# Kernel tuning notes

Hardware: AMD Instinct MI355X
Metric: run time of the kernel (lower is better)

Reference implementation:

```python
import jax, jax.numpy as jnp
import numpy as np

B, T, C, H = 32, 576, 1024, 16
D = C // H  # head_dim = 64

def setup_inputs() -> dict:
    key = jax.random.key(0)
    ks = jax.random.split(key, 5)
    s = 1.0 / np.sqrt(C)
    return {
        "emb_img": jax.random.normal(ks[0], (B, T, C), dtype=jnp.float32),
        "w_qkv": jax.random.normal(ks[1], (C, 3 * C), dtype=jnp.float32) * s,
        "b_qkv": jnp.zeros((3 * C,), dtype=jnp.float32),
        "w_proj": jax.random.normal(ks[2], (C, C), dtype=jnp.float32) * s,
        "b_proj": jnp.zeros((C,), dtype=jnp.float32),
    }

def reference(emb_img, w_qkv, b_qkv, w_proj, b_proj):
    # fused QKV projection
    qkv = emb_img @ w_qkv + b_qkv                       # [B,T,3C]
    q, k, v = jnp.split(qkv, 3, axis=-1)                # each [B,T,C]
    def heads(x):
        return x.reshape(B, T, H, D).transpose(0, 2, 1, 3)  # [B,H,T,D]
    q, k, v = heads(q), heads(k), heads(v)
    # note: original scales by 1/head_dim (not 1/sqrt(head_dim))
    scores = jnp.einsum("bhqd,bhkd->bhqk", q, k) * (1.0 / D)
    causal = jnp.tril(jnp.ones((T, T), dtype=bool))
    scores = jnp.where(causal[None, None], scores, -jnp.inf)
    att = jax.nn.softmax(scores, axis=-1)               # [B,H,T,T]
    y = jnp.einsum("bhqk,bhkd->bhqd", att, v)           # [B,H,T,D]
    y = y.transpose(0, 2, 1, 3).reshape(B, T, C)
    return y @ w_proj + b_proj
```

## Files before the change

kernel.cpp:

```cpp
#include <hip/hip_runtime.h>
#include <stdint.h>

namespace {

constexpr int kB = 32, kT = 576, kC = 1024, kH = 16, kD = 64;
constexpr int kM = kB * kT;
constexpr int kNqkv = 3 * kC;

typedef uint16_t u16;
typedef __attribute__((ext_vector_type(4))) float f32x4;
typedef __attribute__((ext_vector_type(8))) short short8;
typedef __attribute__((ext_vector_type(8))) __bf16 bf16x8;
typedef __attribute__((ext_vector_type(4))) uint16_t u16x4;

#define VMCNT(n) asm volatile("s_waitcnt vmcnt(" #n ")" ::: "memory")

__device__ __forceinline__ f32x4 mfma_bf16(short8 a, short8 b, f32x4 c) {
  return __builtin_amdgcn_mfma_f32_16x16x32_bf16(
      __builtin_bit_cast(bf16x8, a), __builtin_bit_cast(bf16x8, b), c, 0, 0, 0);
}

__device__ __forceinline__ u16 to_bf16(float x) {
  uint32_t u = __float_as_uint(x);
  u += 0x7fffu + ((u >> 16) & 1u);
  return (u16)(u >> 16);
}

__device__ __forceinline__ void gload_lds16(const void* g, void* l) {
  __builtin_amdgcn_global_load_lds(
      (const __attribute__((address_space(1))) uint32_t*)(uintptr_t)g,
      (__attribute__((address_space(3))) uint32_t*)(uintptr_t)l,
      16, 0, 0);
}

__device__ __forceinline__ void bar() {
  asm volatile("" ::: "memory");
  __builtin_amdgcn_s_barrier();
  asm volatile("" ::: "memory");
}

__global__ __launch_bounds__(256) void cvt_bf16_kernel(
    const float* __restrict__ in, u16* __restrict__ out, int n4) {
  const int i = blockIdx.x * 256 + threadIdx.x;
  if (i >= n4) return;
  const f32x4 v = ((const f32x4*)in)[i];
  u16x4 o;
#pragma unroll
  for (int j = 0; j < 4; ++j) o[j] = to_bf16(v[j]);
  ((u16x4*)out)[i] = o;
}

__global__ void tconv_kernel(const float* __restrict__ in, u16* __restrict__ out,
                             int K, int N) {
  __shared__ u16 tile[32][33];
  const int nb = blockIdx.x * 32;
  const int kb = blockIdx.y * 32;
  const int tx = threadIdx.x;
  const int ty = threadIdx.y;
#pragma unroll
  for (int i = 0; i < 32; i += 8)
    tile[ty + i][tx] = to_bf16(in[(size_t)(kb + ty + i) * N + nb + tx]);
  __syncthreads();
#pragma unroll
  for (int i = 0; i < 32; i += 8)
    out[(size_t)(nb + ty + i) * K + kb + tx] = tile[tx][ty + i];
}

__global__ __launch_bounds__(512, 2) void gemm_qkv(
    const u16* __restrict__ A, const u16* __restrict__ Bt,
    const float* __restrict__ bias,
    u16* __restrict__ outQ, u16* __restrict__ outK, u16* __restrict__ outVT) {
  constexpr int Kc = 1024;
  constexpr int NT = Kc / 64;
  __shared__ char lds[3][49152];

  const int tid = threadIdx.x;
  const int wave = tid >> 6;
  const int lane = tid & 63;
  const int lo = lane & 15;
  const int hi = lane >> 4;
  const int wr = wave >> 2;
  const int wc = wave & 3;

  const int lin = blockIdx.x + blockIdx.y * 24;
  const int l2 = (lin & 7) * 216 + (lin >> 3);
  const int n0 = (l2 % 24) * 128;
  const int m0 = (l2 / 24) * 256;

  const u16* srcA[4];
  const u16* srcB[2];
#pragma unroll
  for (int c = 0; c < 4; ++c) {
    const int b = c * 8192 + wave * 1024 + lane * 16;
    const int row = b >> 7;
    const int colb = (b & 127) ^ ((row & 7) << 4);
    srcA[c] = A + (size_t)(m0 + row) * Kc + (colb >> 1);
  }
#pragma unroll
  for (int c = 0; c < 2; ++c) {
    const int b = c * 8192 + wave * 1024 + lane * 16;
    const int row = b >> 7;
    const int colb = (b & 127) ^ ((row & 7) << 4);
    srcB[c] = Bt + (size_t)(n0 + row) * Kc + (colb >> 1);
  }

  auto stage = [&](int slot, int t) {
    const int k0 = t * 64;
    char* base = &lds[slot][0];
#pragma unroll
    for (int c = 0; c < 4; ++c)
      gload_lds16(srcA[c] + k0, base + c * 8192 + wave * 1024);
#pragma unroll
    for (int c = 0; c < 2; ++c)
      gload_lds16(srcB[c] + k0, base + 32768 + c * 8192 + wave * 1024);
  };

  f32x4 acc[8][2] = {};

  auto compute = [&](int slot) {
    const char* base = &lds[slot][0];
    __builtin_amdgcn_s_setprio(1);
#pragma unroll
    for (int ks = 0; ks < 2; ++ks) {
      const int cb = (ks * 64 + hi * 16) ^ ((lo & 7) << 4);
      short8 af[8], bfv[2];
#pragma unroll
      for (int i = 0; i < 8; ++i)
        af[i] = *(const short8*)(base + (wr * 128 + i * 16 + lo) * 128 + cb);
#pragma unroll
      for (int j = 0; j < 2; ++j)
        bfv[j] = *(const short8*)(base + 32768 + (wc * 32 + j * 16 + lo) * 128 + cb);
#pragma unroll
      for (int i = 0; i < 8; ++i)
#pragma unroll
        for (int j = 0; j < 2; ++j)
          acc[i][j] = mfma_bf16(af[i], bfv[j], acc[i][j]);
    }
    __builtin_amdgcn_s_setprio(0);
  };

  stage(0, 0);
  stage(1, 1);
  for (int t = 0; t < NT - 2; ++t) {
    stage((t + 2) % 3, t + 2);
    VMCNT(12);
    bar();
    compute(t % 3);
    bar();
  }
  VMCNT(6);
  bar();
  compute((NT - 2) % 3);
  bar();
  VMCNT(0);
  bar();
  compute((NT - 1) % 3);

  if (n0 >= 2048) {
    bar();
    u16* wlds = (u16*)&lds[0][0] + wave * (32 * 132);
    uint32_t* wlds32 = (uint32_t*)wlds;
#pragma unroll
    for (int j = 0; j < 2; ++j) {
      const int n = n0 + wc * 32 + j * 16 + lo;
      const float bv = bias[n];
#pragma unroll
      for (int i = 0; i < 8; ++i)
#pragma unroll
        for (int rp = 0; rp < 2; ++rp) {
          const u16 w0 = to_bf16(acc[i][j][rp * 2] + bv);
          const u16 w1 = to_bf16(acc[i][j][rp * 2 + 1] + bv);
          wlds32[(j * 16 + lo) * 66 + i * 8 + hi * 2 + rp] =
              (uint32_t)w0 | ((uint32_t)w1 << 16);
        }
    }
    const int l32 = lane & 31;
    const int lh = lane >> 5;
#pragma unroll
    for (int p = 0; p < 16; ++p) {
      const int d_local = p * 2 + lh;
      const int n = n0 + wc * 32 + d_local;
      const int c = n & 1023;
      const int hh = c >> 6;
      const int d = c & 63;
      const int m = m0 + wr * 128 + l32 * 4;
      const int bb = m / kT;
      const int t = m - bb * kT;
      const u16x4 v = *(const u16x4*)&wlds[d_local * 132 + l32 * 4];
      *(u16x4*)&outVT[((size_t)(bb * kH + hh) * kD + d) * kT + t] = v;
    }
  } else {
#pragma unroll
    for (int j = 0; j < 2; ++j) {
      const int n = n0 + wc * 32 + j * 16 + lo;
      const float bv = bias[n];
      const int which = n >> 10;
      const int c = n & 1023;
      const int hh = c >> 6;
      const int d = c & 63;
#pragma unroll
      for (int i = 0; i < 8; ++i) {
        const int mrow = m0 + wr * 128 + i * 16 + hi * 4;
#pragma unroll
        for (int r = 0; r < 4; ++r) {
          const int m = mrow + r;
          const int bb = m / kT;
          const int t = m - bb * kT;
          const float v = acc[i][j][r] + bv;
          if (which == 0)
            outQ[((size_t)(bb * kH + hh) * kT + t) * kD + d] = to_bf16(v * (1.0f / 64.0f));
          else
            outK[((size_t)(bb * kH + hh) * kT + t) * kD + d] = to_bf16(v);
        }
      }
    }
  }
}

__global__ __launch_bounds__(256, 3) void gemm_proj(
    const u16* __restrict__ A, const u16* __restrict__ Bt,
    const float* __restrict__ bias, float* __restrict__ outF) {
  constexpr int Kc = 1024;
  constexpr int NT = Kc / 32;
  __shared__ char lds[3][16384];

  const int tid = threadIdx.x;
  const int wave = tid >> 6;
  const int lane = tid & 63;
  const int lo = lane & 15;
  const int hi = lane >> 4;
  const int wr = wave >> 1;
  const int wc = wave & 1;

  const int lin = blockIdx.x + blockIdx.y * 8;
  const int l2 = (lin & 7) * 144 + (lin >> 3);
  const int n0 = (l2 & 7) * 128;
  const int m0 = (l2 >> 3) * 128;

  const u16* srcA[2];
  const u16* srcB[2];
#pragma unroll
  for (int c = 0; c < 2; ++c) {
    const int off = c * 4096 + tid * 16;
    const int p = off >> 7;
    const int col = (off & 127) ^ ((p & 7) << 4);
    const int r_ = (col < 64) ? p : p + 64;
    const int k_ = (col & 63) >> 1;
    srcA[c] = A + (size_t)(m0 + r_) * Kc + k_;
    srcB[c] = Bt + (size_t)(n0 + r_) * Kc + k_;
  }

  auto stage = [&](int slot, int t) {
    char* base = &lds[slot][0];
#pragma unroll
    for (int c = 0; c < 2; ++c) {
      gload_lds16(srcA[c] + t * 32, base + c * 4096 + wave * 1024);
      gload_lds16(srcB[c] + t * 32, base + 8192 + c * 4096 + wave * 1024);
    }
  };

  f32x4 acc[4][4] = {};

  auto compute = [&](int slot) {
    const char* base = &lds[slot][0];
    const char* baseB = base + 8192;
    const int swz = (lo & 7) << 4;
    short8 af[4], bf[4];
#pragma unroll
    for (int i = 0; i < 4; ++i)
      af[i] = *(const short8*)(base + (i * 16 + lo) * 128 + ((wr * 64 + hi * 16) ^ swz));
#pragma unroll
    for (int j = 0; j < 4; ++j)
      bf[j] = *(const short8*)(baseB + (j * 16 + lo) * 128 + ((wc * 64 + hi * 16) ^ swz));
    __builtin_amdgcn_s_setprio(1);
#pragma unroll
    for (int i = 0; i < 4; ++i)
#pragma unroll
      for (int j = 0; j < 4; ++j)
        acc[i][j] = mfma_bf16(af[i], bf[j], acc[i][j]);
    __builtin_amdgcn_s_setprio(0);
  };

  stage(0, 0);
  stage(1, 1);
  for (int t = 0; t < NT - 2; ++t) {
    stage((t + 2) % 3, t + 2);
    VMCNT(8);
    bar();
    compute(t % 3);
    bar();
  }
  VMCNT(4);
  bar();
  compute((NT - 2) % 3);
  bar();
  VMCNT(0);
  bar();
  compute((NT - 1) % 3);

#pragma unroll
  for (int j = 0; j < 4; ++j) {
    const int n = n0 + wc * 64 + j * 16 + lo;
    const float bv = bias[n];
#pragma unroll
    for (int i = 0; i < 4; ++i) {
      const int mrow = m0 + wr * 64 + i * 16 + hi * 4;
#pragma unroll
      for (int r = 0; r < 4; ++r)
        outF[(size_t)(mrow + r) * kC + n] = acc[i][j][r] + bv;
    }
  }
}

__global__ __launch_bounds__(256) void attn_kernel(
    const u16* __restrict__ Q, const u16* __restrict__ K,
    const u16* __restrict__ VT, u16* __restrict__ Y) {
  __shared__ u16 P[4][32][72];

  const int bh = blockIdx.y;
  const int wave = threadIdx.x >> 6;
  const int lane = threadIdx.x & 63;
  const int lo = lane & 15;
  const int hi = lane >> 4;
  const int q0 = blockIdx.x * 128 + wave * 32;
  if (q0 >= kT) return;

  const u16* Qb = Q + (size_t)bh * kT * kD;
  const u16* Kb = K + (size_t)bh * kT * kD;
  const u16* Vb = VT + (size_t)bh * kD * kT;

  short8 qf[2][2];
#pragma unroll
  for (int h = 0; h < 2; ++h) {
    const u16* qp = Qb + (q0 + h * 16 + lo) * kD + hi * 8;
    qf[h][0] = *(const short8*)qp;
    qf[h][1] = *(const short8*)(qp + 32);
  }

  f32x4 acc[2][4] = {};
  float mrun[2][4], lrun[2][4];
#pragma unroll
  for (int h = 0; h < 2; ++h)
#pragma unroll
    for (int r = 0; r < 4; ++r) { mrun[h][r] = -3e38f; lrun[h][r] = 0.f; }

  const int kv_end = q0 + 32;
  for (int kv = 0; kv < kv_end; kv += 64) {
    f32x4 s[2][4];
#pragma unroll
    for (int kc = 0; kc < 4; ++kc) {
      const u16* kp = Kb + (kv + kc * 16 + lo) * kD + hi * 8;
      const short8 kf0 = *(const short8*)kp;
      const short8 kf1 = *(const short8*)(kp + 32);
#pragma unroll
      for (int h = 0; h < 2; ++h) {
        f32x4 z = {0.f, 0.f, 0.f, 0.f};
        z = mfma_bf16(qf[h][0], kf0, z);
        z = mfma_bf16(qf[h][1], kf1, z);
        s[h][kc] = z;
      }
    }
    if (kv + 63 > q0) {
#pragma unroll
      for (int h = 0; h < 2; ++h)
#pragma unroll
        for (int kc = 0; kc < 4; ++kc)
#pragma unroll
          for (int r = 0; r < 4; ++r)
            if (kv + kc * 16 + lo > q0 + h * 16 + hi * 4 + r) s[h][kc][r] = -3e38f;
    }
#pragma unroll
    for (int h = 0; h < 2; ++h) {
      float pm[4], rs[4], corr[4];
#pragma unroll
      for (int r = 0; r < 4; ++r)
        pm[r] = fmaxf(fmaxf(s[h][0][r], s[h][1][r]), fmaxf(s[h][2][r], s[h][3][r]));
#pragma unroll
      for (int off = 8; off >= 1; off >>= 1)
#pragma unroll
        for (int r = 0; r < 4; ++r) pm[r] = fmaxf(pm[r], __shfl_xor(pm[r], off));
#pragma unroll
      for (int r = 0; r < 4; ++r) {
        const float mnew = fmaxf(mrun[h][r], pm[r]);
        corr[r] = __expf(mrun[h][r] - mnew);
        mrun[h][r] = mnew;
      }
#pragma unroll
      for (int r = 0; r < 4; ++r) {
        float acc_rs = 0.f;
#pragma unroll
        for (int kc = 0; kc < 4; ++kc) {
          const float pv = __expf(s[h][kc][r] - mrun[h][r]);
          acc_rs += pv;
          P[wave][h * 16 + hi * 4 + r][kc * 16 + lo] = to_bf16(pv);
        }
        rs[r] = acc_rs;
      }
#pragma unroll
      for (int off = 8; off >= 1; off >>= 1)
#pragma unroll
        for (int r = 0; r < 4; ++r) rs[r] += __shfl_xor(rs[r], off);
#pragma unroll
      for (int r = 0; r < 4; ++r) lrun[h][r] = lrun[h][r] * corr[r] + rs[r];
#pragma unroll
      for (int nt = 0; nt < 4; ++nt)
#pragma unroll
        for (int r = 0; r < 4; ++r) acc[h][nt][r] *= corr[r];
    }
    short8 pf[2][2];
#pragma unroll
    for (int h = 0; h < 2; ++h) {
      pf[h][0] = *(const short8*)&P[wave][h * 16 + lo][hi * 8];
      pf[h][1] = *(const short8*)&P[wave][h * 16 + lo][32 + hi * 8];
    }
#pragma unroll
    for (int nt = 0; nt < 4; ++nt) {
      const u16* vp = Vb + (nt * 16 + lo) * kT + kv + hi * 8;
      const short8 vf0 = *(const short8*)vp;
      const short8 vf1 = *(const short8*)(vp + 32);
#pragma unroll
      for (int h = 0; h < 2; ++h) {
        acc[h][nt] = mfma_bf16(pf[h][0], vf0, acc[h][nt]);
        acc[h][nt] = mfma_bf16(pf[h][1], vf1, acc[h][nt]);
      }
    }
  }

  const int b = bh >> 4, hh = bh & 15;
#pragma unroll
  for (int h = 0; h < 2; ++h)
#pragma unroll
    for (int r = 0; r < 4; ++r) {
      const float inv = 1.0f / lrun[h][r];
      const int t = q0 + h * 16 + hi * 4 + r;
      const size_t base = ((size_t)(b * kT + t) * kH + hh) * kD;
#pragma unroll
      for (int nt = 0; nt < 4; ++nt)
        Y[base + nt * 16 + lo] = to_bf16(acc[h][nt][r] * inv);
    }
}

}

extern "C" void kernel_launch(void* const* d_in, const int* in_sizes, int n_in,
                              void* d_out, int out_size, void* d_ws, size_t ws_size,
                              hipStream_t stream) {
  (void)in_sizes; (void)n_in; (void)out_size; (void)ws_size;
  const float* emb   = (const float*)d_in[0];
  const float* wqkv  = (const float*)d_in[1];
  const float* bqkv  = (const float*)d_in[2];
  const float* wproj = (const float*)d_in[3];
  const float* bproj = (const float*)d_in[4];
  float* out = (float*)d_out;

  char* p = (char*)d_ws;
  u16* embb   = (u16*)p; p += (size_t)kM * kC * 2;
  u16* wqkvt  = (u16*)p; p += (size_t)kNqkv * kC * 2;
  u16* wprojt = (u16*)p; p += (size_t)kC * kC * 2;
  u16* Qh     = (u16*)p; p += (size_t)kM * kC * 2;
  u16* Kh     = (u16*)p; p += (size_t)kM * kC * 2;
  u16* VTh    = (u16*)p; p += (size_t)kM * kC * 2;
  u16* Yh     = (u16*)p; p += (size_t)kM * kC * 2;

  const int n4 = kM * kC / 4;
  cvt_bf16_kernel<<<dim3((n4 + 255) / 256), 256, 0, stream>>>(emb, embb, n4);
  tconv_kernel<<<dim3(kNqkv / 32, kC / 32), dim3(32, 8), 0, stream>>>(wqkv, wqkvt, kC, kNqkv);
  tconv_kernel<<<dim3(kC / 32, kC / 32), dim3(32, 8), 0, stream>>>(wproj, wprojt, kC, kC);
  gemm_qkv<<<dim3(kNqkv / 128, kM / 256), 512, 0, stream>>>(
      embb, wqkvt, bqkv, Qh, Kh, VTh);
  attn_kernel<<<dim3((kT + 127) / 128, kB * kH), 256, 0, stream>>>(Qh, Kh, VTh, Yh);
  gemm_proj<<<dim3(kC / 128, kM / 128), 256, 0, stream>>>(
      Yh, wprojt, bproj, out);
}
```

Baseline: 371.0 us.

## Restructure attention: transposed scores, exp2 softmax, K/V prefetch, heavy-first scheduling

Reworks the attention kernel in several ways. It computes S^T (K as the A operand), so each lane owns one query row and the row max/sum need only two cross-lane shuffles. The log2(e) factor is folded into the Q scale so exp2 can be used directly. Next-tile K fragments and current V fragments are loaded before the softmax to hide load latency, and the grid is flattened so the longest causal query blocks launch first. In exchange it uses more registers for the prefetched fragments and changes the P write pattern to LDS.

```diff
diff --git a/kernel.cpp b/kernel.cpp
--- a/kernel.cpp
+++ b/kernel.cpp
@@ -6,6 +6,7 @@
 constexpr int kB = 32, kT = 576, kC = 1024, kH = 16, kD = 64;
 constexpr int kM = kB * kT;
 constexpr int kNqkv = 3 * kC;
+constexpr float kQScale = 1.4426950408889634f / 64.0f;
 
 typedef uint16_t u16;
 typedef __attribute__((ext_vector_type(4))) float f32x4;
@@ -14,6 +15,10 @@
 typedef __attribute__((ext_vector_type(4))) uint16_t u16x4;
 
 #define VMCNT(n) asm volatile("s_waitcnt vmcnt(" #n ")" ::: "memory")
+
+__device__ __forceinline__ float fexp2(float x) {
+  return __builtin_amdgcn_exp2f(x);
+}
 
 __device__ __forceinline__ f32x4 mfma_bf16(short8 a, short8 b, f32x4 c) {
   return __builtin_amdgcn_mfma_f32_16x16x32_bf16(
@@ -208,7 +213,7 @@
           const int t = m - bb * kT;
           const float v = acc[i][j][r] + bv;
           if (which == 0)
-            outQ[((size_t)(bb * kH + hh) * kT + t) * kD + d] = to_bf16(v * (1.0f / 64.0f));
+            outQ[((size_t)(bb * kH + hh) * kT + t) * kD + d] = to_bf16(v * kQScale);
           else
             outK[((size_t)(bb * kH + hh) * kT + t) * kD + d] = to_bf16(v);
         }
@@ -317,12 +322,14 @@
     const u16* __restrict__ VT, u16* __restrict__ Y) {
   __shared__ u16 P[4][32][72];
 
-  const int bh = blockIdx.y;
+  const int idx = blockIdx.x;
+  const int qi = 4 - (idx >> 9);
+  const int bh = idx & 511;
   const int wave = threadIdx.x >> 6;
   const int lane = threadIdx.x & 63;
   const int lo = lane & 15;
   const int hi = lane >> 4;
-  const int q0 = blockIdx.x * 128 + wave * 32;
+  const int q0 = qi * 128 + wave * 32;
   if (q0 >= kT) return;
 
   const u16* Qb = Q + (size_t)bh * kT * kD;
@@ -338,74 +345,84 @@
   }
 
   f32x4 acc[2][4] = {};
-  float mrun[2][4], lrun[2][4];
-#pragma unroll
-  for (int h = 0; h < 2; ++h)
-#pragma unroll
-    for (int r = 0; r < 4; ++r) { mrun[h][r] = -3e38f; lrun[h][r] = 0.f; }
+  float mrun[2] = {-3e38f, -3e38f};
+  float lsum[2] = {0.f, 0.f};
+
+  short8 kf[4][2];
+#pragma unroll
+  for (int kc = 0; kc < 4; ++kc) {
+    const u16* kp = Kb + (kc * 16 + lo) * kD + hi * 8;
+    kf[kc][0] = *(const short8*)kp;
+    kf[kc][1] = *(const short8*)(kp + 32);
+  }
 
   const int kv_end = q0 + 32;
   for (int kv = 0; kv < kv_end; kv += 64) {
     f32x4 s[2][4];
 #pragma unroll
-    for (int kc = 0; kc < 4; ++kc) {
-      const u16* kp = Kb + (kv + kc * 16 + lo) * kD + hi * 8;
-      const short8 kf0 = *(const short8*)kp;
-      const short8 kf1 = *(const short8*)(kp + 32);
+    for (int kc = 0; kc < 4; ++kc)
 #pragma unroll
       for (int h = 0; h < 2; ++h) {
         f32x4 z = {0.f, 0.f, 0.f, 0.f};
-        z = mfma_bf16(qf[h][0], kf0, z);
-        z = mfma_bf16(qf[h][1], kf1, z);
+        z = mfma_bf16(kf[kc][0], qf[h][0], z);
+        z = mfma_bf16(kf[kc][1], qf[h][1], z);
         s[h][kc] = z;
       }
+    short8 vf[4][2];
+#pragma unroll
+    for (int nt = 0; nt < 4; ++nt) {
+      const u16* vp = Vb + (nt * 16 + lo) * kT + kv + hi * 8;
+      vf[nt][0] = *(const short8*)vp;
+      vf[nt][1] = *(const short8*)(vp + 32);
+    }
+    if (kv + 64 < kv_end) {
+#pragma unroll
+      for (int kc = 0; kc < 4; ++kc) {
+        const u16* kp = Kb + (kv + 64 + kc * 16 + lo) * kD + hi * 8;
+        kf[kc][0] = *(const short8*)kp;
+        kf[kc][1] = *(const short8*)(kp + 32);
+      }
     }
     if (kv + 63 > q0) {
 #pragma unroll
-      for (int h = 0; h < 2; ++h)
+      for (int h = 0; h < 2; ++h) {
+        const int q = q0 + h * 16 + lo;
 #pragma unroll
         for (int kc = 0; kc < 4; ++kc)
 #pragma unroll
           for (int r = 0; r < 4; ++r)
-            if (kv + kc * 16 + lo > q0 + h * 16 + hi * 4 + r) s[h][kc][r] = -3e38f;
+            if (kv + kc * 16 + hi * 4 + r > q) s[h][kc][r] = -3e38f;
+      }
     }
 #pragma unroll
     for (int h = 0; h < 2; ++h) {
-      float pm[4], rs[4], corr[4];
-#pragma unroll
-      for (int r = 0; r < 4; ++r)
-        pm[r] = fmaxf(fmaxf(s[h][0][r], s[h][1][r]), fmaxf(s[h][2][r], s[h][3][r]));
-#pragma unroll
-      for (int off = 8; off >= 1; off >>= 1)
-#pragma unroll
-        for (int r = 0; r < 4; ++r) pm[r] = fmaxf(pm[r], __shfl_xor(pm[r], off));
-#pragma unroll
-      for (int r = 0; r < 4; ++r) {
-        const float mnew = fmaxf(mrun[h][r], pm[r]);
-        corr[r] = __expf(mrun[h][r] - mnew);
-        mrun[h][r] = mnew;
-      }
-#pragma unroll
-      for (int r = 0; r < 4; ++r) {
-        float acc_rs = 0.f;
-#pragma unroll
-        for (int kc = 0; kc < 4; ++kc) {
-          const float pv = __expf(s[h][kc][r] - mrun[h][r]);
-          acc_rs += pv;
-          P[wave][h * 16 + hi * 4 + r][kc * 16 + lo] = to_bf16(pv);
+      float m01 = fmaxf(fmaxf(s[h][0][0], s[h][0][1]), fmaxf(s[h][0][2], s[h][0][3]));
+      float m23 = fmaxf(fmaxf(s[h][1][0], s[h][1][1]), fmaxf(s[h][1][2], s[h][1][3]));
+      float m45 = fmaxf(fmaxf(s[h][2][0], s[h][2][1]), fmaxf(s[h][2][2], s[h][2][3]));
+      float m67 = fmaxf(fmaxf(s[h][3][0], s[h][3][1]), fmaxf(s[h][3][2], s[h][3][3]));
+      float pm = fmaxf(fmaxf(m01, m23), fmaxf(m45, m67));
+      pm = fmaxf(pm, __shfl_xor(pm, 16));
+      pm = fmaxf(pm, __shfl_xor(pm, 32));
+      const float mnew = fmaxf(mrun[h], pm);
+      const float corr = fexp2(mrun[h] - mnew);
+      mrun[h] = mnew;
+      float psum = 0.f;
+#pragma unroll
+      for (int kc = 0; kc < 4; ++kc) {
+        u16x4 pk;
+#pragma unroll
+        for (int r = 0; r < 4; ++r) {
+          const float pv = fexp2(s[h][kc][r] - mnew);
+          psum += pv;
+          pk[r] = to_bf16(pv);
         }
-        rs[r] = acc_rs;
-      }
-#pragma unroll
-      for (int off = 8; off >= 1; off >>= 1)
-#pragma unroll
-        for (int r = 0; r < 4; ++r) rs[r] += __shfl_xor(rs[r], off);
-#pragma unroll
-      for (int r = 0; r < 4; ++r) lrun[h][r] = lrun[h][r] * corr[r] + rs[r];
+        *(u16x4*)&P[wave][h * 16 + lo][kc * 16 + hi * 4] = pk;
+      }
+      lsum[h] = lsum[h] * corr + psum;
 #pragma unroll
       for (int nt = 0; nt < 4; ++nt)
 #pragma unroll
-        for (int r = 0; r < 4; ++r) acc[h][nt][r] *= corr[r];
+        for (int r = 0; r < 4; ++r) acc[h][nt][r] *= corr;
     }
     short8 pf[2][2];
 #pragma unroll
@@ -414,29 +431,30 @@
       pf[h][1] = *(const short8*)&P[wave][h * 16 + lo][32 + hi * 8];
     }
 #pragma unroll
-    for (int nt = 0; nt < 4; ++nt) {
-      const u16* vp = Vb + (nt * 16 + lo) * kT + kv + hi * 8;
-      const short8 vf0 = *(const short8*)vp;
-      const short8 vf1 = *(const short8*)(vp + 32);
+    for (int nt = 0; nt < 4; ++nt)
 #pragma unroll
       for (int h = 0; h < 2; ++h) {
-        acc[h][nt] = mfma_bf16(pf[h][0], vf0, acc[h][nt]);
-        acc[h][nt] = mfma_bf16(pf[h][1], vf1, acc[h][nt]);
-      }
-    }
-  }
-
+        acc[h][nt] = mfma_bf16(pf[h][0], vf[nt][0], acc[h][nt]);
+        acc[h][nt] = mfma_bf16(pf[h][1], vf[nt][1], acc[h][nt]);
+      }
+  }
+
+#pragma unroll
+  for (int h = 0; h < 2; ++h) {
+    lsum[h] += __shfl_xor(lsum[h], 16);
+    lsum[h] += __shfl_xor(lsum[h], 32);
+  }
   const int b = bh >> 4, hh = bh & 15;
 #pragma unroll
   for (int h = 0; h < 2; ++h)
 #pragma unroll
     for (int r = 0; r < 4; ++r) {
-      const float inv = 1.0f / lrun[h][r];
+      const float linv = 1.0f / __shfl(lsum[h], hi * 4 + r);
       const int t = q0 + h * 16 + hi * 4 + r;
       const size_t base = ((size_t)(b * kT + t) * kH + hh) * kD;
 #pragma unroll
       for (int nt = 0; nt < 4; ++nt)
-        Y[base + nt * 16 + lo] = to_bf16(acc[h][nt][r] * inv);
+        Y[base + nt * 16 + lo] = to_bf16(acc[h][nt][r] * linv);
     }
 }
 
@@ -468,7 +486,7 @@
   tconv_kernel<<<dim3(kC / 32, kC / 32), dim3(32, 8), 0, stream>>>(wproj, wprojt, kC, kC);
   gemm_qkv<<<dim3(kNqkv / 128, kM / 256), 512, 0, stream>>>(
       embb, wqkvt, bqkv, Qh, Kh, VTh);
-  attn_kernel<<<dim3((kT + 127) / 128, kB * kH), 256, 0, stream>>>(Qh, Kh, VTh, Yh);
+  attn_kernel<<<dim3(5 * kB * kH), 256, 0, stream>>>(Qh, Kh, VTh, Yh);
   gemm_proj<<<dim3(kC / 128, kM / 128), 256, 0, stream>>>(
       Yh, wprojt, bproj, out);
 }
```

Measured after the change: 319.0 us. 1.16x faster.
